# Optimization experiments

Hardware: AMD Instinct MI355X
Metric: run time of the kernel (lower is better)

## Reference

```python
import jax, jax.numpy as jnp
import numpy as np

N, C_IN, C_OUT, J = 4096, 256, 256, 2
ATT_SLICE = C_OUT * J  # 512
DENSITY = 0.01
NEG_FILL = -1e20


def _sparse_lap(key, n):
    k1, k2 = jax.random.split(key)
    vals = jax.random.normal(k1, (n, n), dtype=jnp.float32)
    mask = jax.random.uniform(k2, (n, n)) < DENSITY
    return vals * mask + jnp.eye(n, dtype=jnp.float32)


def setup_inputs() -> dict:
    key = jax.random.key(0)
    ks = jax.random.split(key, 12)
    s = 0.05
    return {
        "x": jax.random.normal(ks[0], (N, C_IN), dtype=jnp.float32),
        "Lup": _sparse_lap(ks[1], N),
        "Ld": _sparse_lap(ks[2], N),
        "P": _sparse_lap(ks[3], N),
        "Wirr_w": jax.random.normal(ks[4], (J, C_OUT, C_IN), dtype=jnp.float32) * s,
        "Wirr_b": jax.random.normal(ks[5], (J, C_OUT), dtype=jnp.float32) * s,
        "Wsol_w": jax.random.normal(ks[6], (J, C_OUT, C_IN), dtype=jnp.float32) * s,
        "Wsol_b": jax.random.normal(ks[7], (J, C_OUT), dtype=jnp.float32) * s,
        "Whar_w": jax.random.normal(ks[8], (C_OUT, C_IN), dtype=jnp.float32) * s,
        "Whar_b": jax.random.normal(ks[9], (C_OUT,), dtype=jnp.float32) * s,
        "att_irr": jax.random.normal(ks[10], (2 * ATT_SLICE, 1), dtype=jnp.float32) * s,
        "att_sol": jax.random.normal(ks[11], (2 * ATT_SLICE, 1), dtype=jnp.float32) * s,
    }


def _branch(x, L, Ww, Wb, att):
    # x_cat = concat_j(Linear_j(x)) : [N, J*C_OUT]
    x_cat = (jnp.einsum('nc,jdc->njd', x, Ww) + Wb).reshape(x.shape[0], -1)
    src = x_cat @ att[:ATT_SLICE, :]   # [N,1]
    dst = x_cat @ att[ATT_SLICE:, :]   # [N,1]
    E = jax.nn.leaky_relu(src + dst.T, negative_slope=0.01)  # [N,N]
    E = jnp.where(L != 0, E, NEG_FILL)
    alpha = jax.nn.softmax(E, axis=-1)
    z = (alpha @ x) @ Ww[0].T + Wb[0]
    for p in range(1, J):  # Laplacian-power diffusion
        alpha = alpha @ L
        z = z + (alpha @ x) @ Ww[p].T + Wb[p]
    return z


def reference(x, Lup, Ld, P, Wirr_w, Wirr_b, Wsol_w, Wsol_b, Whar_w, Whar_b, att_irr, att_sol):
    z_i = _branch(x, Ld, Wirr_w, Wirr_b, att_irr)
    z_s = _branch(x, Lup, Wsol_w, Wsol_b, att_sol)
    z_har = (P @ x) @ Whar_w.T + Whar_b
    return z_i + z_s + z_har
```

## Files before the change

### kernel.cpp

```cpp
#include <hip/hip_runtime.h>

#define NROW 4096
#define CH   256
#define MAXNNZ 128

typedef short  short8  __attribute__((ext_vector_type(8)));
typedef unsigned short ushort8 __attribute__((ext_vector_type(8)));
typedef float  f32x4   __attribute__((ext_vector_type(4)));

__device__ inline unsigned short f2bf(float f) {
  unsigned u = __float_as_uint(f);
  return (unsigned short)((u + 0x7fffu + ((u >> 16) & 1u)) >> 16);
}
__device__ inline float bf2f(unsigned short h) {
  return __uint_as_float((unsigned)h << 16);
}
__device__ inline int mbcnt64(unsigned long long m, int base) {
  int t = __builtin_amdgcn_mbcnt_lo((unsigned)m, (unsigned)base);
  return __builtin_amdgcn_mbcnt_hi((unsigned)(m >> 32), t);
}

__global__ void cvt_all(const float* __restrict__ x, const float* __restrict__ Wi,
                        const float* __restrict__ Ws, const float* __restrict__ Wh,
                        unsigned short* __restrict__ xbf, unsigned short* __restrict__ Bbf) {
  int i = blockIdx.x * 256 + threadIdx.x;
  const float* src; unsigned short* dst; int o;
  if (i < 262144)        { src = x;  dst = xbf;          o = i; }
  else if (i < 294912)   { src = Wi; dst = Bbf;          o = i - 262144; }
  else if (i < 327680)   { src = Ws; dst = Bbf + 131072; o = i - 294912; }
  else                   { src = Wh; dst = Bbf + 262144; o = i - 327680; }
  float4 v = ((const float4*)src)[o];
  ushort4 u;
  u.x = f2bf(v.x); u.y = f2bf(v.y); u.z = f2bf(v.z); u.w = f2bf(v.w);
  ((ushort4*)dst)[o] = u;
}

__global__ __launch_bounds__(256) void scan_gemm(
    const float* __restrict__ L0, const float* __restrict__ L1,
    const float* __restrict__ L2, int* __restrict__ idx,
    float* __restrict__ val, int* __restrict__ cnt,
    const unsigned short* __restrict__ A, const unsigned short* __restrict__ Bt,
    unsigned short* __restrict__ Y) {
  __shared__ __align__(16) union {
    struct { unsigned short sA[64 * 64]; unsigned short sB[64 * 64]; } g;
    struct { int sj[4][MAXNNZ]; float sv[4][MAXNNZ]; int scnt[4]; } c;
  } u;
  const int bid = blockIdx.x, tid = threadIdx.x;
  const bool is_gemm = (bid < 12800) && (bid % 10 == 9);

  if (is_gemm) {
    const int gid = bid / 10;
    const int m0 = (gid & 63) * 64, n0 = (gid >> 6) * 64;
    const int wid = tid >> 6, lane = tid & 63;
    const int wr = wid >> 1, wc = wid & 1, lr = lane & 15, kg = lane >> 4;
    f32x4 acc[2][2] = {};
#pragma unroll
    for (int kh = 0; kh < 4; ++kh) {
      {
        for (int c = 0; c < 2; ++c) {
          int chunk = c * 256 + tid;
          int r  = chunk >> 3;
          int cb = (chunk & 7) * 16;
          int cbs = cb ^ ((r & 7) << 4);
          ushort8 va = *(const ushort8*)((const char*)A  + (size_t)(m0 + r) * 512 + kh * 128 + cb);
          *(ushort8*)((char*)u.g.sA + r * 128 + cbs) = va;
          ushort8 vb = *(const ushort8*)((const char*)Bt + (size_t)(n0 + r) * 512 + kh * 128 + cb);
          *(ushort8*)((char*)u.g.sB + r * 128 + cbs) = vb;
        }
      }
      __syncthreads();
#pragma unroll
      for (int ks = 0; ks < 2; ++ks) {
        int kb = ks * 64 + kg * 16;
        short8 a0, a1, b0, b1;
        { int r = wr * 32 + lr;      a0 = *(const short8*)((const char*)u.g.sA + r * 128 + (kb ^ ((r & 7) << 4))); }
        { int r = wr * 32 + 16 + lr; a1 = *(const short8*)((const char*)u.g.sA + r * 128 + (kb ^ ((r & 7) << 4))); }
        { int r = wc * 32 + lr;      b0 = *(const short8*)((const char*)u.g.sB + r * 128 + (kb ^ ((r & 7) << 4))); }
        { int r = wc * 32 + 16 + lr; b1 = *(const short8*)((const char*)u.g.sB + r * 128 + (kb ^ ((r & 7) << 4))); }
        acc[0][0] = __builtin_amdgcn_mfma_f32_16x16x32_bf16(a0, b0, acc[0][0], 0, 0, 0);
        acc[0][1] = __builtin_amdgcn_mfma_f32_16x16x32_bf16(a0, b1, acc[0][1], 0, 0, 0);
        acc[1][0] = __builtin_amdgcn_mfma_f32_16x16x32_bf16(a1, b0, acc[1][0], 0, 0, 0);
        acc[1][1] = __builtin_amdgcn_mfma_f32_16x16x32_bf16(a1, b1, acc[1][1], 0, 0, 0);
      }
      __syncthreads();
    }
#pragma unroll
    for (int mi = 0; mi < 2; ++mi)
#pragma unroll
      for (int ni = 0; ni < 2; ++ni) {
        int col = n0 + wc * 32 + ni * 16 + lr;
#pragma unroll
        for (int r4 = 0; r4 < 4; ++r4) {
          int row = m0 + wr * 32 + mi * 16 + kg * 4 + r4;
          Y[(size_t)row * 1280 + col] = f2bf(acc[mi][ni][r4]);
        }
      }
  } else {
    const int cid = (bid < 12800) ? (bid - (bid + 1) / 10) : (bid - 1280);
    const int mat = cid >> 12, row = cid & 4095;
    const float* L = (mat == 0) ? L0 : (mat == 1) ? L1 : L2;
    const int wi = tid >> 6, lane = tid & 63;
    const f32x4* Lseg = (const f32x4*)(L + (size_t)row * NROW) + wi * 256;

    f32x4 v0 = __builtin_nontemporal_load(Lseg + lane);
    f32x4 v1 = __builtin_nontemporal_load(Lseg + 64 + lane);
    f32x4 v2 = __builtin_nontemporal_load(Lseg + 128 + lane);
    f32x4 v3 = __builtin_nontemporal_load(Lseg + 192 + lane);

    int base = 0;
#define PROCQ(q, cb) {                                                          \
    bool a0 = q[0] != 0.f, a1 = q[1] != 0.f, a2 = q[2] != 0.f, a3 = q[3] != 0.f; \
    unsigned long long b0 = __ballot(a0), b1 = __ballot(a1);                    \
    unsigned long long b2 = __ballot(a2), b3 = __ballot(a3);                    \
    int off = mbcnt64(b3, mbcnt64(b2, mbcnt64(b1, mbcnt64(b0, base))));         \
    if (a0) { if (off < MAXNNZ) { u.c.sj[wi][off] = (cb);     u.c.sv[wi][off] = q[0]; } ++off; } \
    if (a1) { if (off < MAXNNZ) { u.c.sj[wi][off] = (cb) + 1; u.c.sv[wi][off] = q[1]; } ++off; } \
    if (a2) { if (off < MAXNNZ) { u.c.sj[wi][off] = (cb) + 2; u.c.sv[wi][off] = q[2]; } ++off; } \
    if (a3) { if (off < MAXNNZ) { u.c.sj[wi][off] = (cb) + 3; u.c.sv[wi][off] = q[3]; } ++off; } \
    base += __popcll(b0) + __popcll(b1) + __popcll(b2) + __popcll(b3); }
    int colb = wi * 1024 + lane * 4;
    PROCQ(v0, colb)
    PROCQ(v1, colb + 256)
    PROCQ(v2, colb + 512)
    PROCQ(v3, colb + 768)
#undef PROCQ
    if (lane == 0) u.c.scnt[wi] = base < MAXNNZ ? base : MAXNNZ;
    __syncthreads();

    int c0 = u.c.scnt[0], c1 = u.c.scnt[1], c2 = u.c.scnt[2], c3 = u.c.scnt[3];
    int total = c0 + c1 + c2 + c3;
    if (total > MAXNNZ) total = MAXNNZ;
    size_t rbase = ((size_t)mat * NROW + row) * MAXNNZ;
    int t = tid;
    if (t < total) {
      int s, o;
      if      (t < c0)           { s = 0; o = t; }
      else if (t < c0 + c1)      { s = 1; o = t - c0; }
      else if (t < c0 + c1 + c2) { s = 2; o = t - c0 - c1; }
      else                       { s = 3; o = t - c0 - c1 - c2; }
      idx[rbase + t] = u.c.sj[s][o];
      val[rbase + t] = u.c.sv[s][o];
    }
    if (t == 0) cnt[mat * NROW + row] = total;
  }
}

__global__ __launch_bounds__(256) void spmm_sdv(
    const int* __restrict__ idx, const float* __restrict__ val,
    const int* __restrict__ cnt, const float* __restrict__ ai,
    const float* __restrict__ as_, const float* __restrict__ bi,
    const float* __restrict__ bs, unsigned short* __restrict__ Y,
    float* __restrict__ sdv) {
  int row = blockIdx.x, t = threadIdx.x, w = t >> 6, l = t & 63;
  __shared__ float satt[2048];
  __shared__ float red2[8];
  __shared__ float sbias[4];
  __shared__ int   sj0[MAXNNZ], sj1[MAXNNZ];
  __shared__ float sv0[MAXNNZ], sv1[MAXNNZ];
  __shared__ float part[4][256];

  for (int k = t; k < 1024; k += 256) { satt[k] = ai[k]; satt[1024 + k] = as_[k]; }
  {
    const float* av = (w & 2) ? as_ : ai;
    const float* bv = (w & 2) ? bs : bi;
    int off = (w & 1) * 512;
    float b = 0.f;
    for (int k = l; k < 512; k += 64) b += av[off + k] * bv[k];
    for (int o = 32; o; o >>= 1) b += __shfl_xor(b, o);
    if (l == 0) sbias[w] = b;
  }
  int n0 = cnt[row], n1 = cnt[NROW + row];
  if (t < n0) { sj0[t] = idx[(size_t)row * MAXNNZ + t];          sv0[t] = val[(size_t)row * MAXNNZ + t]; }
  if (t < n1) { sj1[t] = idx[((size_t)NROW + row) * MAXNNZ + t]; sv1[t] = val[((size_t)NROW + row) * MAXNNZ + t]; }
  ushort4 y4 = *(const ushort4*)(Y + (size_t)row * 1280 + 4 * t);
  __syncthreads();

  {
    int c0 = 4 * t;
    int aoff = (t < 128) ? 0 : 1024;
    int cc = c0 & 511;
    float sp = satt[aoff + cc]       * bf2f(y4.x) + satt[aoff + cc + 1]       * bf2f(y4.y)
             + satt[aoff + cc + 2]   * bf2f(y4.z) + satt[aoff + cc + 3]       * bf2f(y4.w);
    float dp = satt[aoff + 512 + cc] * bf2f(y4.x) + satt[aoff + 512 + cc + 1] * bf2f(y4.y)
             + satt[aoff + 512 + cc + 2] * bf2f(y4.z) + satt[aoff + 512 + cc + 3] * bf2f(y4.w);
    for (int o = 32; o; o >>= 1) { sp += __shfl_xor(sp, o); dp += __shfl_xor(dp, o); }
    if (l == 0) { red2[w * 2] = sp; red2[w * 2 + 1] = dp; }
  }

  float4 acc0 = {0.f, 0.f, 0.f, 0.f}, acc1 = {0.f, 0.f, 0.f, 0.f};
  for (int k = w; k < n0; k += 4) {
    ushort4 y = *(const ushort4*)(Y + (size_t)sj0[k] * 1280 + 256 + 4 * l);
    float a = sv0[k];
    acc0.x += a * bf2f(y.x); acc0.y += a * bf2f(y.y);
    acc0.z += a * bf2f(y.z); acc0.w += a * bf2f(y.w);
  }
  for (int k = w; k < n1; k += 4) {
    ushort4 y = *(const ushort4*)(Y + (size_t)sj1[k] * 1280 + 768 + 4 * l);
    float a = sv1[k];
    acc1.x += a * bf2f(y.x); acc1.y += a * bf2f(y.y);
    acc1.z += a * bf2f(y.z); acc1.w += a * bf2f(y.w);
  }
  ((float4*)part[w])[l] = acc0;
  __syncthreads();
  if (t == 0) {
    sdv[row]            = red2[0] + red2[2] + sbias[0];
    sdv[NROW + row]     = red2[1] + red2[3] + sbias[1];
    sdv[2 * NROW + row] = red2[4] + red2[6] + sbias[2];
    sdv[3 * NROW + row] = red2[5] + red2[7] + sbias[3];
  }
  if (t < 64) {
    unsigned short* yp = Y + (size_t)row * 1280 + 4 * t;
    ushort4 yb = *(const ushort4*)yp;
    ushort4 o;
    o.x = f2bf(bf2f(yb.x) + part[0][4 * t]     + part[1][4 * t]     + part[2][4 * t]     + part[3][4 * t]);
    o.y = f2bf(bf2f(yb.y) + part[0][4 * t + 1] + part[1][4 * t + 1] + part[2][4 * t + 1] + part[3][4 * t + 1]);
    o.z = f2bf(bf2f(yb.z) + part[0][4 * t + 2] + part[1][4 * t + 2] + part[2][4 * t + 2] + part[3][4 * t + 2]);
    o.w = f2bf(bf2f(yb.w) + part[0][4 * t + 3] + part[1][4 * t + 3] + part[2][4 * t + 3] + part[3][4 * t + 3]);
    *(ushort4*)yp = o;
  }
  __syncthreads();
  ((float4*)part[w])[l] = acc1;
  __syncthreads();
  if (t < 64) {
    unsigned short* yp = Y + (size_t)row * 1280 + 512 + 4 * t;
    ushort4 yb = *(const ushort4*)yp;
    ushort4 o;
    o.x = f2bf(bf2f(yb.x) + part[0][4 * t]     + part[1][4 * t]     + part[2][4 * t]     + part[3][4 * t]);
    o.y = f2bf(bf2f(yb.y) + part[0][4 * t + 1] + part[1][4 * t + 1] + part[2][4 * t + 1] + part[3][4 * t + 1]);
    o.z = f2bf(bf2f(yb.z) + part[0][4 * t + 2] + part[1][4 * t + 2] + part[2][4 * t + 2] + part[3][4 * t + 2]);
    o.w = f2bf(bf2f(yb.w) + part[0][4 * t + 3] + part[1][4 * t + 3] + part[2][4 * t + 3] + part[3][4 * t + 3]);
    *(ushort4*)yp = o;
  }
}

__global__ __launch_bounds__(256) void final_z(const int* __restrict__ idx,
                        const float* __restrict__ val, const int* __restrict__ cnt,
                        const float* __restrict__ sdv,
                        const unsigned short* __restrict__ Y,
                        const float* __restrict__ bi, const float* __restrict__ bs,
                        const float* __restrict__ bh, float* __restrict__ Z) {
  int row = blockIdx.x, t = threadIdx.x, w = t >> 6, l = t & 63;
  __shared__ float sa[MAXNNZ];
  __shared__ int   sj[MAXNNZ];
  __shared__ float red[4];
  __shared__ float part[4][256];
  float4 acc = {0.f, 0.f, 0.f, 0.f};

  for (int br = 0; br < 2; ++br) {
    size_t rbase = ((size_t)br * NROW + row) * MAXNNZ;
    int n = cnt[br * NROW + row];
    const float* srcv = sdv + (2 * br) * NROW;
    const float* dstv = sdv + (2 * br + 1) * NROW;
    float e = -1e30f;
    if (t < n) {
      int j = idx[rbase + t];
      sj[t] = j;
      float v = srcv[row] + dstv[j];
      e = v >= 0.f ? v : 0.01f * v;
    }
    float m = e;
    for (int o = 32; o; o >>= 1) m = fmaxf(m, __shfl_xor(m, o));
    if ((t & 63) == 0) red[t >> 6] = m;
    __syncthreads();
    m = fmaxf(fmaxf(red[0], red[1]), fmaxf(red[2], red[3]));
    __syncthreads();
    float p = (t < n) ? expf(e - m) : 0.f;
    float s = p;
    for (int o = 32; o; o >>= 1) s += __shfl_xor(s, o);
    if ((t & 63) == 0) red[t >> 6] = s;
    __syncthreads();
    s = red[0] + red[1] + red[2] + red[3];
    if (t < n) sa[t] = p / s;
    __syncthreads();
    int cd = br ? 512 : 0;
    for (int k = w; k < n; k += 4) {
      ushort4 y = *(const ushort4*)(Y + (size_t)sj[k] * 1280 + cd + 4 * l);
      float a = sa[k];
      acc.x += a * bf2f(y.x); acc.y += a * bf2f(y.y);
      acc.z += a * bf2f(y.z); acc.w += a * bf2f(y.w);
    }
    __syncthreads();
  }

  {
    size_t rbase = ((size_t)2 * NROW + row) * MAXNNZ;
    int n = cnt[2 * NROW + row];
    if (t < n) { sj[t] = idx[rbase + t]; sa[t] = val[rbase + t]; }
    __syncthreads();
    for (int k = w; k < n; k += 4) {
      ushort4 y = *(const ushort4*)(Y + (size_t)sj[k] * 1280 + 1024 + 4 * l);
      float a = sa[k];
      acc.x += a * bf2f(y.x); acc.y += a * bf2f(y.y);
      acc.z += a * bf2f(y.z); acc.w += a * bf2f(y.w);
    }
  }
  ((float4*)part[w])[l] = acc;
  __syncthreads();
  if (t < 64) {
    float4 r;
    int c = 4 * t;
    r.x = part[0][c]     + part[1][c]     + part[2][c]     + part[3][c]     + bi[c]     + bi[256 + c] + bs[c]     + bs[256 + c] + bh[c];
    r.y = part[0][c + 1] + part[1][c + 1] + part[2][c + 1] + part[3][c + 1] + bi[c + 1] + bi[257 + c] + bs[c + 1] + bs[257 + c] + bh[c + 1];
    r.z = part[0][c + 2] + part[1][c + 2] + part[2][c + 2] + part[3][c + 2] + bi[c + 2] + bi[258 + c] + bs[c + 2] + bs[258 + c] + bh[c + 2];
    r.w = part[0][c + 3] + part[1][c + 3] + part[2][c + 3] + part[3][c + 3] + bi[c + 3] + bi[259 + c] + bs[c + 3] + bs[259 + c] + bh[c + 3];
    *(float4*)(Z + (size_t)row * 256 + c) = r;
  }
}

extern "C" void kernel_launch(void* const* d_in, const int* in_sizes, int n_in,
                              void* d_out, int out_size, void* d_ws, size_t ws_size,
                              hipStream_t stream) {
  const float* x      = (const float*)d_in[0];
  const float* Lup    = (const float*)d_in[1];
  const float* Ld     = (const float*)d_in[2];
  const float* P      = (const float*)d_in[3];
  const float* Wirr_w = (const float*)d_in[4];
  const float* Wirr_b = (const float*)d_in[5];
  const float* Wsol_w = (const float*)d_in[6];
  const float* Wsol_b = (const float*)d_in[7];
  const float* Whar_w = (const float*)d_in[8];
  const float* Whar_b = (const float*)d_in[9];
  const float* att_i  = (const float*)d_in[10];
  const float* att_s  = (const float*)d_in[11];
  float* Z = (float*)d_out;

  char* w = (char*)d_ws;
  auto alloc = [&](size_t bytes) { void* p = (void*)w; w += (bytes + 255) & ~(size_t)255; return p; };

  int*   idx  = (int*)alloc((size_t)3 * NROW * MAXNNZ * 4);
  float* val  = (float*)alloc((size_t)3 * NROW * MAXNNZ * 4);
  int*   cnt  = (int*)alloc((size_t)3 * NROW * 4);
  float* sdv  = (float*)alloc(4 * NROW * 4);
  unsigned short* xbf = (unsigned short*)alloc((size_t)NROW * CH * 2);
  unsigned short* Bbf = (unsigned short*)alloc((size_t)1280 * CH * 2);
  unsigned short* Y   = (unsigned short*)alloc((size_t)NROW * 1280 * 2);

  cvt_all<<<(262144 + 32768 + 32768 + 16384) / 256, 256, 0, stream>>>(x, Wirr_w, Wsol_w, Whar_w, xbf, Bbf);

  scan_gemm<<<13568, 256, 0, stream>>>(Ld, Lup, P, idx, val, cnt, xbf, Bbf, Y);

  spmm_sdv<<<NROW, 256, 0, stream>>>(idx, val, cnt, att_i, att_s, Wirr_b, Wsol_b, Y, sdv);

  final_z<<<NROW, 256, 0, stream>>>(idx, val, cnt, sdv, Y, Wirr_b, Wsol_b, Whar_b, Z);
}
```

Baseline: 116.1 us.

## Split fused scan+GEMM kernel into separate scan and MFMA GEMM launches

Replaces the combined kernel, which interleaved GEMM blocks among Laplacian-scan blocks, with two kernels: a dedicated sparse-row compaction scan and a standalone bf16 MFMA GEMM. The scan is launched first, ahead of the bf16 conversion. This removes per-block branching and the shared-memory union, and lets each kernel keep its own resource footprint. It gives up the overlap of GEMM compute with the memory-bound scan and adds one more launch.

After: 114.9 us. About the same (-1.0%).

```diff
diff --git a/kernel.cpp b/kernel.cpp
--- a/kernel.cpp
+++ b/kernel.cpp
@@ -18,6 +18,61 @@
 __device__ inline int mbcnt64(unsigned long long m, int base) {
   int t = __builtin_amdgcn_mbcnt_lo((unsigned)m, (unsigned)base);
   return __builtin_amdgcn_mbcnt_hi((unsigned)(m >> 32), t);
+}
+
+__global__ __launch_bounds__(256) void scan_nt(
+    const float* __restrict__ L0, const float* __restrict__ L1,
+    const float* __restrict__ L2, int* __restrict__ idx,
+    float* __restrict__ val, int* __restrict__ cnt) {
+  __shared__ int   sj[4][MAXNNZ];
+  __shared__ float sv[4][MAXNNZ];
+  __shared__ int   scnt[4];
+  const int cid = blockIdx.x;
+  const int mat = cid >> 12, row = cid & 4095;
+  const float* L = (mat == 0) ? L0 : (mat == 1) ? L1 : L2;
+  const int wi = threadIdx.x >> 6, lane = threadIdx.x & 63;
+  const f32x4* Lseg = (const f32x4*)(L + (size_t)row * NROW) + wi * 256;
+
+  f32x4 v0 = __builtin_nontemporal_load(Lseg + lane);
+  f32x4 v1 = __builtin_nontemporal_load(Lseg + 64 + lane);
+  f32x4 v2 = __builtin_nontemporal_load(Lseg + 128 + lane);
+  f32x4 v3 = __builtin_nontemporal_load(Lseg + 192 + lane);
+
+  int base = 0;
+#define PROCQ(q, cb) {                                                          \
+    bool a0 = q[0] != 0.f, a1 = q[1] != 0.f, a2 = q[2] != 0.f, a3 = q[3] != 0.f; \
+    unsigned long long b0 = __ballot(a0), b1 = __ballot(a1);                    \
+    unsigned long long b2 = __ballot(a2), b3 = __ballot(a3);                    \
+    int off = mbcnt64(b3, mbcnt64(b2, mbcnt64(b1, mbcnt64(b0, base))));         \
+    if (a0) { if (off < MAXNNZ) { sj[wi][off] = (cb);     sv[wi][off] = q[0]; } ++off; } \
+    if (a1) { if (off < MAXNNZ) { sj[wi][off] = (cb) + 1; sv[wi][off] = q[1]; } ++off; } \
+    if (a2) { if (off < MAXNNZ) { sj[wi][off] = (cb) + 2; sv[wi][off] = q[2]; } ++off; } \
+    if (a3) { if (off < MAXNNZ) { sj[wi][off] = (cb) + 3; sv[wi][off] = q[3]; } ++off; } \
+    base += __popcll(b0) + __popcll(b1) + __popcll(b2) + __popcll(b3); }
+  int colb = wi * 1024 + lane * 4;
+  PROCQ(v0, colb)
+  PROCQ(v1, colb + 256)
+  PROCQ(v2, colb + 512)
+  PROCQ(v3, colb + 768)
+#undef PROCQ
+  if (lane == 0) scnt[wi] = base < MAXNNZ ? base : MAXNNZ;
+  __syncthreads();
+
+  int c0 = scnt[0], c1 = scnt[1], c2 = scnt[2], c3 = scnt[3];
+  int total = c0 + c1 + c2 + c3;
+  if (total > MAXNNZ) total = MAXNNZ;
+  size_t rbase = ((size_t)mat * NROW + row) * MAXNNZ;
+  int t = threadIdx.x;
+  if (t < total) {
+    int s, o;
+    if      (t < c0)           { s = 0; o = t; }
+    else if (t < c0 + c1)      { s = 1; o = t - c0; }
+    else if (t < c0 + c1 + c2) { s = 2; o = t - c0 - c1; }
+    else                       { s = 3; o = t - c0 - c1 - c2; }
+    idx[rbase + t] = sj[s][o];
+    val[rbase + t] = sv[s][o];
+  }
+  if (t == 0) cnt[mat * NROW + row] = total;
 }
 
 __global__ void cvt_all(const float* __restrict__ x, const float* __restrict__ Wi,
@@ -35,114 +90,55 @@
   ((ushort4*)dst)[o] = u;
 }
 
-__global__ __launch_bounds__(256) void scan_gemm(
-    const float* __restrict__ L0, const float* __restrict__ L1,
-    const float* __restrict__ L2, int* __restrict__ idx,
-    float* __restrict__ val, int* __restrict__ cnt,
+__global__ __launch_bounds__(256) void gemm_mfma(
     const unsigned short* __restrict__ A, const unsigned short* __restrict__ Bt,
     unsigned short* __restrict__ Y) {
-  __shared__ __align__(16) union {
-    struct { unsigned short sA[64 * 64]; unsigned short sB[64 * 64]; } g;
-    struct { int sj[4][MAXNNZ]; float sv[4][MAXNNZ]; int scnt[4]; } c;
-  } u;
-  const int bid = blockIdx.x, tid = threadIdx.x;
-  const bool is_gemm = (bid < 12800) && (bid % 10 == 9);
-
-  if (is_gemm) {
-    const int gid = bid / 10;
-    const int m0 = (gid & 63) * 64, n0 = (gid >> 6) * 64;
-    const int wid = tid >> 6, lane = tid & 63;
-    const int wr = wid >> 1, wc = wid & 1, lr = lane & 15, kg = lane >> 4;
-    f32x4 acc[2][2] = {};
-#pragma unroll
-    for (int kh = 0; kh < 4; ++kh) {
-      {
-        for (int c = 0; c < 2; ++c) {
-          int chunk = c * 256 + tid;
-          int r  = chunk >> 3;
-          int cb = (chunk & 7) * 16;
-          int cbs = cb ^ ((r & 7) << 4);
-          ushort8 va = *(const ushort8*)((const char*)A  + (size_t)(m0 + r) * 512 + kh * 128 + cb);
-          *(ushort8*)((char*)u.g.sA + r * 128 + cbs) = va;
-          ushort8 vb = *(const ushort8*)((const char*)Bt + (size_t)(n0 + r) * 512 + kh * 128 + cb);
-          *(ushort8*)((char*)u.g.sB + r * 128 + cbs) = vb;
-        }
+  __shared__ __align__(16) unsigned short sA[64 * 64];
+  __shared__ __align__(16) unsigned short sB[64 * 64];
+  const int gid = blockIdx.x, tid = threadIdx.x;
+  const int m0 = (gid & 63) * 64, n0 = (gid >> 6) * 64;
+  const int wid = tid >> 6, lane = tid & 63;
+  const int wr = wid >> 1, wc = wid & 1, lr = lane & 15, kg = lane >> 4;
+  f32x4 acc[2][2] = {};
+#pragma unroll
+  for (int kh = 0; kh < 4; ++kh) {
+    for (int c = 0; c < 2; ++c) {
+      int chunk = c * 256 + tid;
+      int r  = chunk >> 3;
+      int cb = (chunk & 7) * 16;
+      int cbs = cb ^ ((r & 7) << 4);
+      ushort8 va = *(const ushort8*)((const char*)A  + (size_t)(m0 + r) * 512 + kh * 128 + cb);
+      *(ushort8*)((char*)sA + r * 128 + cbs) = va;
+      ushort8 vb = *(const ushort8*)((const char*)Bt + (size_t)(n0 + r) * 512 + kh * 128 + cb);
+      *(ushort8*)((char*)sB + r * 128 + cbs) = vb;
+    }
+    __syncthreads();
+#pragma unroll
+    for (int ks = 0; ks < 2; ++ks) {
+      int kb = ks * 64 + kg * 16;
+      short8 a0, a1, b0, b1;
+      { int r = wr * 32 + lr;      a0 = *(const short8*)((const char*)sA + r * 128 + (kb ^ ((r & 7) << 4))); }
+      { int r = wr * 32 + 16 + lr; a1 = *(const short8*)((const char*)sA + r * 128 + (kb ^ ((r & 7) << 4))); }
+      { int r = wc * 32 + lr;      b0 = *(const short8*)((const char*)sB + r * 128 + (kb ^ ((r & 7) << 4))); }
+      { int r = wc * 32 + 16 + lr; b1 = *(const short8*)((const char*)sB + r * 128 + (kb ^ ((r & 7) << 4))); }
+      acc[0][0] = __builtin_amdgcn_mfma_f32_16x16x32_bf16(a0, b0, acc[0][0], 0, 0, 0);
+      acc[0][1] = __builtin_amdgcn_mfma_f32_16x16x32_bf16(a0, b1, acc[0][1], 0, 0, 0);
+      acc[1][0] = __builtin_amdgcn_mfma_f32_16x16x32_bf16(a1, b0, acc[1][0], 0, 0, 0);
+      acc[1][1] = __builtin_amdgcn_mfma_f32_16x16x32_bf16(a1, b1, acc[1][1], 0, 0, 0);
+    }
+    __syncthreads();
+  }
+#pragma unroll
+  for (int mi = 0; mi < 2; ++mi)
+#pragma unroll
+    for (int ni = 0; ni < 2; ++ni) {
+      int col = n0 + wc * 32 + ni * 16 + lr;
+#pragma unroll
+      for (int r4 = 0; r4 < 4; ++r4) {
+        int row = m0 + wr * 32 + mi * 16 + kg * 4 + r4;
+        Y[(size_t)row * 1280 + col] = f2bf(acc[mi][ni][r4]);
       }
-      __syncthreads();
-#pragma unroll
-      for (int ks = 0; ks < 2; ++ks) {
-        int kb = ks * 64 + kg * 16;
-        short8 a0, a1, b0, b1;
-        { int r = wr * 32 + lr;      a0 = *(const short8*)((const char*)u.g.sA + r * 128 + (kb ^ ((r & 7) << 4))); }
-        { int r = wr * 32 + 16 + lr; a1 = *(const short8*)((const char*)u.g.sA + r * 128 + (kb ^ ((r & 7) << 4))); }
-        { int r = wc * 32 + lr;      b0 = *(const short8*)((const char*)u.g.sB + r * 128 + (kb ^ ((r & 7) << 4))); }
-        { int r = wc * 32 + 16 + lr; b1 = *(const short8*)((const char*)u.g.sB + r * 128 + (kb ^ ((r & 7) << 4))); }
-        acc[0][0] = __builtin_amdgcn_mfma_f32_16x16x32_bf16(a0, b0, acc[0][0], 0, 0, 0);
-        acc[0][1] = __builtin_amdgcn_mfma_f32_16x16x32_bf16(a0, b1, acc[0][1], 0, 0, 0);
-        acc[1][0] = __builtin_amdgcn_mfma_f32_16x16x32_bf16(a1, b0, acc[1][0], 0, 0, 0);
-        acc[1][1] = __builtin_amdgcn_mfma_f32_16x16x32_bf16(a1, b1, acc[1][1], 0, 0, 0);
-      }
-      __syncthreads();
-    }
-#pragma unroll
-    for (int mi = 0; mi < 2; ++mi)
-#pragma unroll
-      for (int ni = 0; ni < 2; ++ni) {
-        int col = n0 + wc * 32 + ni * 16 + lr;
-#pragma unroll
-        for (int r4 = 0; r4 < 4; ++r4) {
-          int row = m0 + wr * 32 + mi * 16 + kg * 4 + r4;
-          Y[(size_t)row * 1280 + col] = f2bf(acc[mi][ni][r4]);
-        }
-      }
-  } else {
-    const int cid = (bid < 12800) ? (bid - (bid + 1) / 10) : (bid - 1280);
-    const int mat = cid >> 12, row = cid & 4095;
-    const float* L = (mat == 0) ? L0 : (mat == 1) ? L1 : L2;
-    const int wi = tid >> 6, lane = tid & 63;
-    const f32x4* Lseg = (const f32x4*)(L + (size_t)row * NROW) + wi * 256;
-
-    f32x4 v0 = __builtin_nontemporal_load(Lseg + lane);
-    f32x4 v1 = __builtin_nontemporal_load(Lseg + 64 + lane);
-    f32x4 v2 = __builtin_nontemporal_load(Lseg + 128 + lane);
-    f32x4 v3 = __builtin_nontemporal_load(Lseg + 192 + lane);
-
-    int base = 0;
-#define PROCQ(q, cb) {                                                          \
-    bool a0 = q[0] != 0.f, a1 = q[1] != 0.f, a2 = q[2] != 0.f, a3 = q[3] != 0.f; \
-    unsigned long long b0 = __ballot(a0), b1 = __ballot(a1);                    \
-    unsigned long long b2 = __ballot(a2), b3 = __ballot(a3);                    \
-    int off = mbcnt64(b3, mbcnt64(b2, mbcnt64(b1, mbcnt64(b0, base))));         \
-    if (a0) { if (off < MAXNNZ) { u.c.sj[wi][off] = (cb);     u.c.sv[wi][off] = q[0]; } ++off; } \
-    if (a1) { if (off < MAXNNZ) { u.c.sj[wi][off] = (cb) + 1; u.c.sv[wi][off] = q[1]; } ++off; } \
-    if (a2) { if (off < MAXNNZ) { u.c.sj[wi][off] = (cb) + 2; u.c.sv[wi][off] = q[2]; } ++off; } \
-    if (a3) { if (off < MAXNNZ) { u.c.sj[wi][off] = (cb) + 3; u.c.sv[wi][off] = q[3]; } ++off; } \
-    base += __popcll(b0) + __popcll(b1) + __popcll(b2) + __popcll(b3); }
-    int colb = wi * 1024 + lane * 4;
-    PROCQ(v0, colb)
-    PROCQ(v1, colb + 256)
-    PROCQ(v2, colb + 512)
-    PROCQ(v3, colb + 768)
-#undef PROCQ
-    if (lane == 0) u.c.scnt[wi] = base < MAXNNZ ? base : MAXNNZ;
-    __syncthreads();
-
-    int c0 = u.c.scnt[0], c1 = u.c.scnt[1], c2 = u.c.scnt[2], c3 = u.c.scnt[3];
-    int total = c0 + c1 + c2 + c3;
-    if (total > MAXNNZ) total = MAXNNZ;
-    size_t rbase = ((size_t)mat * NROW + row) * MAXNNZ;
-    int t = tid;
-    if (t < total) {
-      int s, o;
-      if      (t < c0)           { s = 0; o = t; }
-      else if (t < c0 + c1)      { s = 1; o = t - c0; }
-      else if (t < c0 + c1 + c2) { s = 2; o = t - c0 - c1; }
-      else                       { s = 3; o = t - c0 - c1 - c2; }
-      idx[rbase + t] = u.c.sj[s][o];
-      val[rbase + t] = u.c.sv[s][o];
-    }
-    if (t == 0) cnt[mat * NROW + row] = total;
-  }
+    }
 }
 
 __global__ __launch_bounds__(256) void spmm_sdv(
@@ -335,9 +331,10 @@
   unsigned short* Bbf = (unsigned short*)alloc((size_t)1280 * CH * 2);
   unsigned short* Y   = (unsigned short*)alloc((size_t)NROW * 1280 * 2);
 
+  scan_nt<<<3 * NROW, 256, 0, stream>>>(Ld, Lup, P, idx, val, cnt);
+
   cvt_all<<<(262144 + 32768 + 32768 + 16384) / 256, 256, 0, stream>>>(x, Wirr_w, Wsol_w, Whar_w, xbf, Bbf);
-
-  scan_gemm<<<13568, 256, 0, stream>>>(Ld, Lup, P, idx, val, cnt, xbf, Bbf, Y);
+  gemm_mfma<<<1280, 256, 0, stream>>>(xbf, Bbf, Y);
 
   spmm_sdv<<<NROW, 256, 0, stream>>>(idx, val, cnt, att_i, att_s, Wirr_b, Wsol_b, Y, sdv);
 
```
